# Kernel tuning notes

Hardware: AMD Instinct MI355X
Metric: run time of the kernel (lower is better)

Reference implementation:

```python
import jax, jax.numpy as jnp
import numpy as np

B, S, D, H = 2, 1024, 1024, 8
HD = D // H            # head_dim = 128
NBUCKETS = 64          # bucket_size (number of hash buckets)
NEG = -1e30


def setup_inputs() -> dict:
    key = jax.random.key(0)
    ks = jax.random.split(key, 10)
    scale = D ** -0.5
    return {
        "x": jax.random.normal(ks[0], (B, S, D), dtype=jnp.float32),
        "Wq": jax.random.normal(ks[1], (D, D), dtype=jnp.float32) * scale,
        "bq": jnp.zeros((D,), dtype=jnp.float32),
        "Wk": jax.random.normal(ks[2], (D, D), dtype=jnp.float32) * scale,
        "bk": jnp.zeros((D,), dtype=jnp.float32),
        "Wv": jax.random.normal(ks[3], (D, D), dtype=jnp.float32) * scale,
        "bv": jnp.zeros((D,), dtype=jnp.float32),
        "Wo": jax.random.normal(ks[4], (D, D), dtype=jnp.float32) * scale,
        "bo": jnp.zeros((D,), dtype=jnp.float32),
        "hash_proj": jax.random.normal(ks[5], (H, HD, NBUCKETS), dtype=jnp.float32),
    }


def reference(x, Wq, bq, Wk, bk, Wv, bv, Wo, bo, hash_proj):
    b, s, d = x.shape
    n = b * s  # buckets gather (batch, token) pairs jointly -> flatten batch into tokens

    def split_heads(y):  # [B,S,D] -> [H, B*S, HD]
        return y.reshape(b, s, H, HD).transpose(2, 0, 1, 3).reshape(H, n, HD)

    q = split_heads(x @ Wq + bq)
    k = split_heads(x @ Wk + bk)
    v = split_heads(x @ Wv + bv)

    # learned LSH routing: argmax over hash projections per head
    hash_scores = jnp.einsum('hnd,hdf->hnf', q, hash_proj)
    buckets = jnp.argmax(hash_scores, axis=-1)  # [H, N] int

    # per-bucket attention == masked dense attention with same-bucket mask
    dots = jnp.einsum('hnd,hmd->hnm', q, k) / (HD ** 0.5)  # [H,N,N]
    same = buckets[:, :, None] == buckets[:, None, :]
    attn = jax.nn.softmax(jnp.where(same, dots, NEG), axis=-1)
    o = jnp.einsum('hnm,hmd->hnd', attn, v)  # [H,N,HD]

    out = o.reshape(H, b, s, HD).transpose(1, 2, 0, 3).reshape(b, s, d)
    return out @ Wo + bo
```

## Files before the change

### kernel.cpp

```cpp
#include <hip/hip_runtime.h>
#include <stdint.h>

typedef __attribute__((ext_vector_type(8))) short short8;
typedef __attribute__((ext_vector_type(4))) short short4v;
typedef __attribute__((ext_vector_type(4))) float float4v;
typedef unsigned short u16;

#define N_TOK 2048
#define D_MODEL 1024
#define N_HEAD 8
#define HDIM 128
#define N_BUCKET 64
#define WL_CAP 2048
#define ATTN_BLOCKS 384

__device__ __forceinline__ u16 f2bf(float f) {
  uint32_t u = __float_as_uint(f);
  uint32_t r = u + 0x7fffu + ((u >> 16) & 1u);
  return (u16)(r >> 16);
}
__device__ __forceinline__ float bf2f(u16 h) {
  return __uint_as_float(((uint32_t)h) << 16);
}

__device__ __forceinline__ void async_load16(const void* g, void* l) {
  __builtin_amdgcn_global_load_lds(
      (const __attribute__((address_space(1))) void*)g,
      (__attribute__((address_space(3))) void*)l, 16, 0, 0);
}

__device__ __forceinline__ int xcd_swz(int bid, int nwg) {
  return (bid & 7) * (nwg >> 3) + (bid >> 3);
}

__global__ __launch_bounds__(256) void prep_kernel(
    const float* __restrict__ x, const float* __restrict__ Wq,
    const float* __restrict__ Wk, const float* __restrict__ Wv,
    const float* __restrict__ Wo, const float* __restrict__ proj,
    u16* __restrict__ xhi, u16* __restrict__ xlo,
    u16* __restrict__ wqt_hi, u16* __restrict__ wqt_lo, u16* __restrict__ kvt,
    u16* __restrict__ wot, u16* __restrict__ projt_hi,
    u16* __restrict__ projt_lo) {
  const int z = blockIdx.z;
  if (z == 4) {
    int base = (blockIdx.y * 32 + blockIdx.x) * 2048 + threadIdx.x * 8;
    float4v a = *(const float4v*)&x[base];
    float4v b = *(const float4v*)&x[base + 4];
    short8 hi, lo;
#pragma unroll
    for (int j = 0; j < 4; j++) {
      u16 h = f2bf(a[j]);
      hi[j] = (short)h;
      lo[j] = (short)f2bf(a[j] - bf2f(h));
    }
#pragma unroll
    for (int j = 0; j < 4; j++) {
      u16 h = f2bf(b[j]);
      hi[4 + j] = (short)h;
      lo[4 + j] = (short)f2bf(b[j] - bf2f(h));
    }
    *(short8*)&xhi[base] = hi;
    *(short8*)&xlo[base] = lo;
    return;
  }
  __shared__ float tile[32][33];
  int tx = threadIdx.x & 31, ty = threadIdx.x >> 5;
  if (z == 5) {
    if (blockIdx.x >= 2) return;
    const int head = blockIdx.y >> 2;
    const int r0 = (blockIdx.y & 3) * 32;
    const int c0 = blockIdx.x * 32;
    const float* in = proj + (size_t)head * 128 * 64;
#pragma unroll
    for (int i = 0; i < 4; i++) {
      int rl = ty + i * 8;
      tile[rl][tx] = in[(size_t)(r0 + rl) * 64 + c0 + tx];
    }
    __syncthreads();
#pragma unroll
    for (int i = 0; i < 4; i++) {
      int cl = ty + i * 8;
      float v = tile[tx][cl];
      size_t oidx = (size_t)head * 64 * 128 + (size_t)(c0 + cl) * 128 + r0 + tx;
      u16 h = f2bf(v);
      projt_hi[oidx] = h;
      projt_lo[oidx] = f2bf(v - bf2f(h));
    }
    return;
  }
  const float* in = (z == 0) ? Wq : (z == 1) ? Wk : (z == 2) ? Wv : Wo;
  u16* hi = (z == 0) ? wqt_hi
            : (z == 1) ? kvt
            : (z == 2) ? (kvt + (size_t)1024 * 1024) : wot;
  u16* lo = (z == 0) ? wqt_lo : nullptr;
  const int C = 1024, R = 1024;
  int c0 = blockIdx.x * 32, r0 = blockIdx.y * 32;
#pragma unroll
  for (int i = 0; i < 4; i++) {
    int rl = ty + i * 8;
    tile[rl][tx] = in[(size_t)(r0 + rl) * C + c0 + tx];
  }
  __syncthreads();
#pragma unroll
  for (int i = 0; i < 4; i++) {
    int cl = ty + i * 8;
    float v = tile[tx][cl];
    size_t oidx = (size_t)(c0 + cl) * R + r0 + tx;
    u16 h = f2bf(v);
    hi[oidx] = h;
    if (lo) lo[oidx] = f2bf(v - bf2f(h));
  }
}

template <int BM>
__device__ __forceinline__ void stage_tiles2(const u16* A, const u16* Bt,
                                             u16* As, u16* Bs, int bm, int bn,
                                             int K, int ko, int wave, int lane) {
  const int arow = lane >> 2;
  const int acolb = (lane & 3) * 16;
  constexpr int ACH = BM / 16;
  constexpr int PC = (ACH + 8) / 4;
#pragma unroll
  for (int cc = 0; cc < PC; cc++) {
    int idx = wave * PC + cc;
    if (idx < ACH) {
      int row = idx * 16 + arow;
      const char* g = (const char*)A + ((size_t)(bm + row) * K + ko) * 2 + acolb;
      async_load16(g, (char*)As + idx * 1024);
    } else {
      int row = (idx - ACH) * 16 + arow;
      const char* g = (const char*)Bt + ((size_t)(bn + row) * K + ko) * 2 + acolb;
      async_load16(g, (char*)Bs + (idx - ACH) * 1024);
    }
  }
}

template <int BM>
__global__ __launch_bounds__(256) void gemm_bf16_kernel(
    const u16* __restrict__ A, const u16* __restrict__ Bt,
    float* __restrict__ C, const float* __restrict__ bias,
    const float* __restrict__ bias2, u16* __restrict__ kbf,
    u16* __restrict__ vbf, int N, int K, int flags) {
  constexpr int MI = BM / 32;
  __shared__ __align__(16) u16 As[2][BM * 32];
  __shared__ __align__(16) u16 Bs[2][128 * 32];
  const int tid = threadIdx.x;
  const int wave = tid >> 6, lane = tid & 63;
  const int lhi = lane >> 4, llo = lane & 15;
  const int nbn = N >> 7;
  const int bid = xcd_swz(blockIdx.x, gridDim.x);
  const int bm = (bid / nbn) * BM;
  const int bn = (bid % nbn) << 7;
  const int wm = (BM == 128) ? (wave >> 1) * 64 : (wave & 1) * 32;
  const int wn = (BM == 128) ? (wave & 1) * 64 : (wave >> 1) * 64;

  float4v acc[MI][4];
#pragma unroll
  for (int mi = 0; mi < MI; mi++)
#pragma unroll
    for (int ni = 0; ni < 4; ni++)
#pragma unroll
      for (int r = 0; r < 4; r++) acc[mi][ni][r] = 0.f;

  stage_tiles2<BM>(A, Bt, As[0], Bs[0], bm, bn, K, 0, wave, lane);
  __syncthreads();
  const int nk = K >> 5;
  for (int t = 0; t < nk; t++) {
    const int cur = t & 1;
    if (t + 1 < nk)
      stage_tiles2<BM>(A, Bt, As[cur ^ 1], Bs[cur ^ 1], bm, bn, K,
                       (t + 1) << 5, wave, lane);
    short8 af[MI], bfr[4];
#pragma unroll
    for (int i = 0; i < MI; i++)
      af[i] = *(const short8*)&As[cur][(wm + i * 16 + llo) * 32 + lhi * 8];
#pragma unroll
    for (int i = 0; i < 4; i++)
      bfr[i] = *(const short8*)&Bs[cur][(wn + i * 16 + llo) * 32 + lhi * 8];
#pragma unroll
    for (int mi = 0; mi < MI; mi++)
#pragma unroll
      for (int ni = 0; ni < 4; ni++)
        acc[mi][ni] = __builtin_amdgcn_mfma_f32_16x16x32_bf16(af[mi], bfr[ni],
                                                              acc[mi][ni], 0, 0, 0);
    __syncthreads();
  }

#pragma unroll
  for (int mi = 0; mi < MI; mi++)
#pragma unroll
    for (int ni = 0; ni < 4; ni++) {
      int row0 = bm + wm + mi * 16 + lhi * 4;
      int col = bn + wn + ni * 16 + llo;
      if (flags & 8) {
        u16* dst = (col < 1024) ? kbf : vbf;
        int c = col & 1023;
        float bb = (col < 1024) ? bias[c] : bias2[c];
#pragma unroll
        for (int r = 0; r < 4; r++)
          dst[(size_t)(row0 + r) * 1024 + c] = f2bf(acc[mi][ni][r] + bb);
      } else {
        float bb = (flags & 2) ? bias[col] : 0.f;
        float* cp = C + (size_t)row0 * N + col;
#pragma unroll
        for (int r = 0; r < 4; r++) cp[(size_t)r * N] = acc[mi][ni][r] + bb;
      }
    }
}

#define QROW 136
__global__ __launch_bounds__(256) void proj_gemm_kernel(
    const u16* __restrict__ A0, const u16* __restrict__ A1,
    const u16* __restrict__ B0, const u16* __restrict__ B1,
    const u16* __restrict__ kvt, const u16* __restrict__ projt_hi,
    const u16* __restrict__ projt_lo, const float* __restrict__ bq,
    const float* __restrict__ bk, const float* __restrict__ bv,
    u16* __restrict__ qbb, int* __restrict__ bucket,
    u16* __restrict__ kbf, u16* __restrict__ vbf) {
  __shared__ __align__(16) u16 S3[2][12288];
  const int tid = threadIdx.x;
  const int wave = tid >> 6, lane = tid & 63;
  const int lhi = lane >> 4, llo = lane & 15;
  const int arow = lane >> 2;
  const int acolb = (lane & 3) * 16;
  const int K = 1024;
  const int b = blockIdx.x;
  const int cls = b % 3;

  if (cls == 0) {
    const int bid = b / 3;
    const int bm = (bid >> 3) * 64;
    const int bn = (bid & 7) << 7;
    const int wm = (wave & 1) * 32;
    const int wn = (wave >> 1) * 64;

    float4v acc[2][4];
#pragma unroll
    for (int mi = 0; mi < 2; mi++)
#pragma unroll
      for (int ni = 0; ni < 4; ni++)
#pragma unroll
        for (int r = 0; r < 4; r++) acc[mi][ni][r] = 0.f;

    auto stage = [&](int bb2, int ko) {
      char* base = (char*)&S3[bb2][0];
#pragma unroll
      for (int cc = 0; cc < 6; cc++) {
        int idx = wave * 6 + cc;
        const u16* src;
        int row;
        char* dst;
        if (idx < 4) {
          src = A0; row = bm + idx * 16 + arow; dst = base + idx * 1024;
        } else if (idx < 8) {
          src = A1; row = bm + (idx - 4) * 16 + arow; dst = base + 4096 + (idx - 4) * 1024;
        } else if (idx < 16) {
          src = B0; row = bn + (idx - 8) * 16 + arow; dst = base + 8192 + (idx - 8) * 1024;
        } else {
          src = B1; row = bn + (idx - 16) * 16 + arow; dst = base + 16384 + (idx - 16) * 1024;
        }
        async_load16((const char*)src + ((size_t)row * K + ko) * 2 + acolb, dst);
      }
    };

    stage(0, 0);
    __syncthreads();
    for (int t = 0; t < 32; t++) {
      const int cur = t & 1;
      if (t + 1 < 32) stage(cur ^ 1, (t + 1) << 5);
      const u16* Sc = &S3[cur][0];
      short8 afh[2], afl[2], bfh[4], bfl[4];
#pragma unroll
      for (int i = 0; i < 2; i++) {
        afh[i] = *(const short8*)&Sc[(wm + i * 16 + llo) * 32 + lhi * 8];
        afl[i] = *(const short8*)&Sc[2048 + (wm + i * 16 + llo) * 32 + lhi * 8];
      }
#pragma unroll
      for (int i = 0; i < 4; i++) {
        bfh[i] = *(const short8*)&Sc[4096 + (wn + i * 16 + llo) * 32 + lhi * 8];
        bfl[i] = *(const short8*)&Sc[8192 + (wn + i * 16 + llo) * 32 + lhi * 8];
      }
#pragma unroll
      for (int mi = 0; mi < 2; mi++)
#pragma unroll
        for (int ni = 0; ni < 4; ni++)
          acc[mi][ni] = __builtin_amdgcn_mfma_f32_16x16x32_bf16(afh[mi], bfh[ni],
                                                                acc[mi][ni], 0, 0, 0);
#pragma unroll
      for (int mi = 0; mi < 2; mi++)
#pragma unroll
        for (int ni = 0; ni < 4; ni++)
          acc[mi][ni] = __builtin_amdgcn_mfma_f32_16x16x32_bf16(afh[mi], bfl[ni],
                                                                acc[mi][ni], 0, 0, 0);
#pragma unroll
      for (int mi = 0; mi < 2; mi++)
#pragma unroll
        for (int ni = 0; ni < 4; ni++)
          acc[mi][ni] = __builtin_amdgcn_mfma_f32_16x16x32_bf16(afl[mi], bfh[ni],
                                                                acc[mi][ni], 0, 0, 0);
      __syncthreads();
    }

    u16* sQh = &S3[0][0];
    u16* sQl = &S3[0][64 * QROW];
#pragma unroll
    for (int mi = 0; mi < 2; mi++)
#pragma unroll
      for (int ni = 0; ni < 4; ni++) {
        int rl0 = wm + mi * 16 + lhi * 4;
        int col = wn + ni * 16 + llo;
        float bb = bq[bn + col];
#pragma unroll
        for (int r = 0; r < 4; r++) {
          float v = acc[mi][ni][r] + bb;
          u16 h = f2bf(v);
          qbb[(size_t)(bm + rl0 + r) * 1024 + bn + col] = h;
          sQh[(rl0 + r) * QROW + col] = h;
          sQl[(rl0 + r) * QROW + col] = f2bf(v - bf2f(h));
        }
      }
    __syncthreads();

    {
      const int h = bn >> 7;
      const int wm2 = wave * 16;
      short8 qh[4], ql[4];
#pragma unroll
      for (int kf = 0; kf < 4; kf++) {
        qh[kf] = *(const short8*)&sQh[(wm2 + llo) * QROW + kf * 32 + lhi * 8];
        ql[kf] = *(const short8*)&sQl[(wm2 + llo) * QROW + kf * 32 + lhi * 8];
      }
      const u16* ph = projt_hi + (size_t)h * 64 * 128;
      const u16* pl = projt_lo + (size_t)h * 64 * 128;
      float4v sc2[4];
#pragma unroll
      for (int nf = 0; nf < 4; nf++)
#pragma unroll
        for (int r = 0; r < 4; r++) sc2[nf][r] = 0.f;
#pragma unroll
      for (int nf = 0; nf < 4; nf++) {
        int brow = (nf * 16 + llo) * 128;
#pragma unroll
        for (int kf = 0; kf < 4; kf++) {
          short8 bh = *(const short8*)&ph[brow + kf * 32 + lhi * 8];
          short8 bl = *(const short8*)&pl[brow + kf * 32 + lhi * 8];
          sc2[nf] = __builtin_amdgcn_mfma_f32_16x16x32_bf16(qh[kf], bh, sc2[nf], 0, 0, 0);
          sc2[nf] = __builtin_amdgcn_mfma_f32_16x16x32_bf16(qh[kf], bl, sc2[nf], 0, 0, 0);
          sc2[nf] = __builtin_amdgcn_mfma_f32_16x16x32_bf16(ql[kf], bh, sc2[nf], 0, 0, 0);
        }
      }
#pragma unroll
      for (int r = 0; r < 4; r++) {
        float best = sc2[0][r];
        int bi = llo;
#pragma unroll
        for (int nf = 1; nf < 4; nf++) {
          float v = sc2[nf][r];
          if (v > best) { best = v; bi = nf * 16 + llo; }
        }
#pragma unroll
        for (int o = 1; o < 16; o <<= 1) {
          float ov = __shfl_xor(best, o);
          int oi = __shfl_xor(bi, o);
          if (ov > best || (ov == best && oi < bi)) { best = ov; bi = oi; }
        }
        if (llo == 0) bucket[h * N_TOK + bm + wm2 + lhi * 4 + r] = bi;
      }
    }
  } else {
    const int bid2 = (b / 3) * 2 + (cls - 1);
    const int bm = (bid2 >> 4) * 64;
    const int bn = (bid2 & 15) << 7;
    const int wm = (wave & 1) * 32;
    const int wn = (wave >> 1) * 64;

    float4v acc[2][4];
#pragma unroll
    for (int mi = 0; mi < 2; mi++)
#pragma unroll
      for (int ni = 0; ni < 4; ni++)
#pragma unroll
        for (int r = 0; r < 4; r++) acc[mi][ni][r] = 0.f;

    stage_tiles2<64>(A0, kvt, &S3[0][0], &S3[0][4096], bm, bn, K, 0, wave, lane);
    __syncthreads();
    for (int t = 0; t < 32; t++) {
      const int cur = t & 1;
      if (t + 1 < 32)
        stage_tiles2<64>(A0, kvt, &S3[0][(cur ^ 1) * 2048],
                         &S3[0][4096 + (cur ^ 1) * 4096], bm, bn, K,
                         (t + 1) << 5, wave, lane);
      const u16* Ac = &S3[0][cur * 2048];
      const u16* Bc = &S3[0][4096 + cur * 4096];
      short8 af[2], bfr[4];
#pragma unroll
      for (int i = 0; i < 2; i++)
        af[i] = *(const short8*)&Ac[(wm + i * 16 + llo) * 32 + lhi * 8];
#pragma unroll
      for (int i = 0; i < 4; i++)
        bfr[i] = *(const short8*)&Bc[(wn + i * 16 + llo) * 32 + lhi * 8];
#pragma unroll
      for (int mi = 0; mi < 2; mi++)
#pragma unroll
        for (int ni = 0; ni < 4; ni++)
          acc[mi][ni] = __builtin_amdgcn_mfma_f32_16x16x32_bf16(af[mi], bfr[ni],
                                                                acc[mi][ni], 0, 0, 0);
      __syncthreads();
    }

#pragma unroll
    for (int mi = 0; mi < 2; mi++)
#pragma unroll
      for (int ni = 0; ni < 4; ni++) {
        int row0 = bm + wm + mi * 16 + lhi * 4;
        int col = bn + wn + ni * 16 + llo;
        u16* dst = (col < 1024) ? kbf : vbf;
        int c = col & 1023;
        float bb = (col < 1024) ? bk[c] : bv[c];
#pragma unroll
        for (int r = 0; r < 4; r++)
          dst[(size_t)(row0 + r) * 1024 + c] = f2bf(acc[mi][ni][r] + bb);
      }
  }
}

__global__ __launch_bounds__(64) void bucket_count_kernel(
    const int* __restrict__ bucket, int* __restrict__ counts) {
  int hb = blockIdx.x;
  int h = hb >> 6, b = hb & 63;
  int lane = threadIdx.x;
  int cnt = 0;
  for (int t = 0; t < N_TOK; t += 64) {
    bool match = bucket[h * N_TOK + t + lane] == b;
    unsigned long long mask = __ballot(match);
    cnt += __popcll(mask);
  }
  if (lane == 0) counts[hb] = cnt;
}

__global__ __launch_bounds__(512) void build_wl_kernel(
    const int* __restrict__ counts, int* __restrict__ offsets,
    int* __restrict__ wl, int* __restrict__ wl_count) {
  __shared__ int sc[512];
  int tid = threadIdx.x;
  int cnt = counts[tid];
  sc[tid] = cnt;
  __syncthreads();
  for (int o = 1; o < 512; o <<= 1) {
    int v = (tid >= o) ? sc[tid - o] : 0;
    __syncthreads();
    sc[tid] += v;
    __syncthreads();
  }
  offsets[tid] = sc[tid] - cnt;
  __syncthreads();
  int nq = (cnt + 15) >> 4;
  sc[tid] = nq;
  __syncthreads();
  for (int o = 1; o < 512; o <<= 1) {
    int v = (tid >= o) ? sc[tid - o] : 0;
    __syncthreads();
    sc[tid] += v;
    __syncthreads();
  }
  int base = sc[tid] - nq;
  int h = tid >> 6, b = tid & 63;
  for (int i = 0; i < nq; i++) wl[base + i] = (h << 13) | (b << 7) | i;
  if (tid == 511) wl_count[0] = sc[511];
}

__global__ __launch_bounds__(64) void bucket_fill_kernel(
    const int* __restrict__ bucket, const int* __restrict__ offsets,
    int* __restrict__ perm) {
  int hb = blockIdx.x;
  int h = hb >> 6, b = hb & 63;
  int lane = threadIdx.x;
  int base = offsets[hb];
  for (int t = 0; t < N_TOK; t += 64) {
    int tok = t + lane;
    bool match = bucket[h * N_TOK + tok] == b;
    unsigned long long mask = __ballot(match);
    if (match) {
      int pos = base + __popcll(mask & ((1ull << lane) - 1ull));
      perm[pos] = tok;
    }
    base += __popcll(mask);
  }
}

__global__ __launch_bounds__(256) void gather_vt_kernel(
    const u16* __restrict__ vbb, const int* __restrict__ perm,
    u16* __restrict__ Vts) {
  __shared__ u16 lds[64][72];
  int bid = blockIdx.x;
  int h = bid >> 6;
  int ptile = (bid & 63) >> 1;
  int d0 = (bid & 1) * 64;
  int pos0 = ptile * 64;
  int t = threadIdx.x;
#pragma unroll
  for (int i = 0; i < 2; i++) {
    int unit = t + 256 * i;
    int p = unit >> 3, seg = unit & 7;
    int tok = perm[h * N_TOK + pos0 + p];
    short8 v = *(const short8*)&vbb[(size_t)tok * D_MODEL + h * HDIM + d0 + seg * 8];
    *(short8*)&lds[p][seg * 8] = v;
  }
  __syncthreads();
#pragma unroll
  for (int i = 0; i < 8; i++) {
    int unit = t + 256 * i;
    int drow = unit >> 5, pp = unit & 31;
    uint32_t val = (uint32_t)lds[2 * pp][drow] |
                   ((uint32_t)lds[2 * pp + 1][drow] << 16);
    uint32_t* dst = (uint32_t*)&Vts[(size_t)(h * HDIM + d0 + drow) * N_TOK + pos0];
    dst[pp] = val;
  }
}

__global__ __launch_bounds__(256) void attn_bucket_kernel(
    const u16* __restrict__ qbb, const u16* __restrict__ kbb,
    const u16* __restrict__ Vts, const int* __restrict__ perm,
    const int* __restrict__ offsets, const int* __restrict__ counts,
    const int* __restrict__ wl, const int* __restrict__ wl_count,
    u16* __restrict__ ob) {
  const int wave = threadIdx.x >> 6, lane = threadIdx.x & 63;
  const int lhi = lane >> 4, llo = lane & 15;
  const int wslot = blockIdx.x * 4 + wave;
  const int NW = ATTN_BLOCKS * 4;
  const int cnt = wl_count[0];
  __shared__ __align__(16) u16 P_lds[4][16][64];
  const float scale = 0.08838834764831845f;

  for (int e = wslot; e < cnt; e += NW) {
    int ent = wl[e];
    int h = ent >> 13, qt = ent & 127;
    int hb = (h << 6) | ((ent >> 7) & 63);
    int off = offsets[hb];
    int bs = counts[hb];
    int offh = off - h * N_TOK;
    int qbase = qt * 16;

    int qr = qbase + llo;
    int tokq = perm[off + min(qr, bs - 1)];
    const u16* qrow = &qbb[(size_t)tokq * D_MODEL + h * HDIM];
    short8 qf[4];
#pragma unroll
    for (int kf = 0; kf < 4; kf++)
      qf[kf] = *(const short8*)&qrow[kf * 32 + lhi * 8];

    float m[4], l[4];
#pragma unroll
    for (int r = 0; r < 4; r++) { m[r] = -INFINITY; l[r] = 0.f; }
    float4v accO[8];
#pragma unroll
    for (int d = 0; d < 8; d++)
#pragma unroll
      for (int r = 0; r < 4; r++) accO[d][r] = 0.f;

    for (int c0 = 0; c0 < bs; c0 += 64) {
      float4v scv[4];
#pragma unroll
      for (int nf = 0; nf < 4; nf++)
#pragma unroll
        for (int r = 0; r < 4; r++) scv[nf][r] = 0.f;
#pragma unroll
      for (int nf = 0; nf < 4; nf++) {
        int kcol = c0 + nf * 16 + llo;
        int tokk = perm[off + min(kcol, bs - 1)];
        const u16* krow = &kbb[(size_t)tokk * D_MODEL + h * HDIM];
#pragma unroll
        for (int kf = 0; kf < 4; kf++) {
          short8 kfr = *(const short8*)&krow[kf * 32 + lhi * 8];
          scv[nf] = __builtin_amdgcn_mfma_f32_16x16x32_bf16(qf[kf], kfr, scv[nf], 0, 0, 0);
        }
      }

      float tmax[4];
#pragma unroll
      for (int r = 0; r < 4; r++) tmax[r] = -INFINITY;
#pragma unroll
      for (int nf = 0; nf < 4; nf++) {
        bool valid = (c0 + nf * 16 + llo) < bs;
#pragma unroll
        for (int r = 0; r < 4; r++) {
          float v = valid ? scv[nf][r] * scale : -1e30f;
          scv[nf][r] = v;
          tmax[r] = fmaxf(tmax[r], v);
        }
      }
#pragma unroll
      for (int r = 0; r < 4; r++)
#pragma unroll
        for (int o = 1; o < 16; o <<= 1)
          tmax[r] = fmaxf(tmax[r], __shfl_xor(tmax[r], o));

      float resc[4], psum[4];
#pragma unroll
      for (int r = 0; r < 4; r++) {
        float mn = fmaxf(m[r], tmax[r]);
        resc[r] = __expf(m[r] - mn);
        m[r] = mn;
        psum[r] = 0.f;
      }
#pragma unroll
      for (int nf = 0; nf < 4; nf++)
#pragma unroll
        for (int r = 0; r < 4; r++) {
          float p = __expf(scv[nf][r] - m[r]);
          psum[r] += p;
          P_lds[wave][lhi * 4 + r][nf * 16 + llo] = f2bf(p);
        }
#pragma unroll
      for (int r = 0; r < 4; r++) {
#pragma unroll
        for (int o = 1; o < 16; o <<= 1) psum[r] += __shfl_xor(psum[r], o);
        l[r] = l[r] * resc[r] + psum[r];
      }
#pragma unroll
      for (int d = 0; d < 8; d++)
#pragma unroll
        for (int r = 0; r < 4; r++) accO[d][r] *= resc[r];

      asm volatile("s_waitcnt lgkmcnt(0)" ::: "memory");
      short8 pf[2];
#pragma unroll
      for (int k2 = 0; k2 < 2; k2++)
        pf[k2] = *(const short8*)&P_lds[wave][llo][k2 * 32 + lhi * 8];
#pragma unroll
      for (int d = 0; d < 8; d++)
#pragma unroll
        for (int k2 = 0; k2 < 2; k2++) {
          short8 vfr = *(const short8*)&Vts[(size_t)(h * HDIM + d * 16 + llo) * N_TOK +
                                            offh + c0 + k2 * 32 + lhi * 8];
          accO[d] = __builtin_amdgcn_mfma_f32_16x16x32_bf16(pf[k2], vfr, accO[d], 0, 0, 0);
        }
      asm volatile("" ::: "memory");
    }

#pragma unroll
    for (int r = 0; r < 4; r++) {
      int rl = qbase + lhi * 4 + r;
      if (rl < bs) {
        int tok = perm[off + rl];
        float inv = 1.f / l[r];
#pragma unroll
        for (int d = 0; d < 8; d++)
          ob[(size_t)tok * D_MODEL + h * HDIM + d * 16 + llo] = f2bf(accO[d][r] * inv);
      }
    }
  }
}

extern "C" void kernel_launch(void* const* d_in, const int* in_sizes, int n_in,
                              void* d_out, int out_size, void* d_ws, size_t ws_size,
                              hipStream_t stream) {
  const float* x  = (const float*)d_in[0];
  const float* Wq = (const float*)d_in[1];
  const float* bq = (const float*)d_in[2];
  const float* Wk = (const float*)d_in[3];
  const float* bk = (const float*)d_in[4];
  const float* Wv = (const float*)d_in[5];
  const float* bv = (const float*)d_in[6];
  const float* Wo = (const float*)d_in[7];
  const float* bo = (const float*)d_in[8];
  const float* hp = (const float*)d_in[9];
  float* out = (float*)d_out;

  char* ws = (char*)d_ws;
  size_t off = 0;
  auto alloc = [&](size_t b) {
    char* p = ws + off;
    off += (b + 255) & ~(size_t)255;
    return p;
  };

  const int N = N_TOK, D = D_MODEL;
  u16* xhi    = (u16*)alloc((size_t)N * D * 2);
  u16* xlo    = (u16*)alloc((size_t)N * D * 2);
  u16* wqt_hi = (u16*)alloc((size_t)D * D * 2);
  u16* wqt_lo = (u16*)alloc((size_t)D * D * 2);
  u16* kvt    = (u16*)alloc((size_t)2 * D * D * 2);
  u16* wot    = (u16*)alloc((size_t)D * D * 2);
  u16* pjt_hi = (u16*)alloc((size_t)N_HEAD * 64 * 128 * 2);
  u16* pjt_lo = (u16*)alloc((size_t)N_HEAD * 64 * 128 * 2);
  u16* qbb    = (u16*)alloc((size_t)N * D * 2);
  u16* kbb    = (u16*)alloc((size_t)N * D * 2);
  u16* vbb    = (u16*)alloc((size_t)N * D * 2);
  u16* Vts    = (u16*)alloc((size_t)N_HEAD * HDIM * N * 2 + 256);
  int* bucket = (int*)alloc((size_t)N_HEAD * N * 4);
  int* counts = (int*)alloc(512 * 4);
  int* offs   = (int*)alloc(512 * 4);
  int* perm   = (int*)alloc((size_t)N_HEAD * N * 4);
  int* wl     = (int*)alloc(WL_CAP * 4);
  int* wlcnt  = (int*)alloc(256);
  u16* ob     = (u16*)alloc((size_t)N * D * 2);

  prep_kernel<<<dim3(32, 32, 6), 256, 0, stream>>>(
      x, Wq, Wk, Wv, Wo, hp, xhi, xlo, wqt_hi, wqt_lo, kvt, wot, pjt_hi, pjt_lo);

  proj_gemm_kernel<<<768, 256, 0, stream>>>(
      xhi, xlo, wqt_hi, wqt_lo, kvt, pjt_hi, pjt_lo, bq, bk, bv,
      qbb, bucket, kbb, vbb);

  bucket_count_kernel<<<512, 64, 0, stream>>>(bucket, counts);
  build_wl_kernel<<<1, 512, 0, stream>>>(counts, offs, wl, wlcnt);
  bucket_fill_kernel<<<512, 64, 0, stream>>>(bucket, offs, perm);
  gather_vt_kernel<<<512, 256, 0, stream>>>(vbb, perm, Vts);

  attn_bucket_kernel<<<ATTN_BLOCKS, 256, 0, stream>>>(
      qbb, kbb, Vts, perm, offs, counts, wl, wlcnt, ob);

  gemm_bf16_kernel<64><<<(N / 64) * (D / 128), 256, 0, stream>>>(
      ob, wot, out, bo, nullptr, nullptr, nullptr, D, D, 2);

  (void)in_sizes; (void)n_in; (void)out_size; (void)ws_size;
}
```

Measured before the change: 109.8 us.

## Fuse bucket counting into projection GEMM and merge scan with bucket fill

Bucket histogram counts are now produced with atomics inside the projection GEMM's argmax epilogue, with the counts zeroed by spare prep blocks. The separate scan and fill kernels are merged into one, where each block computes its own prefix offsets from the 512 counts. This removes two kernel launches and one full pass over the bucket array. In exchange it adds atomic contention and redundant prefix sums in every block.

```diff
diff --git a/kernel.cpp b/kernel.cpp
--- a/kernel.cpp
+++ b/kernel.cpp
@@ -40,7 +40,7 @@
     u16* __restrict__ xhi, u16* __restrict__ xlo,
     u16* __restrict__ wqt_hi, u16* __restrict__ wqt_lo, u16* __restrict__ kvt,
     u16* __restrict__ wot, u16* __restrict__ projt_hi,
-    u16* __restrict__ projt_lo) {
+    u16* __restrict__ projt_lo, int* __restrict__ counts) {
   const int z = blockIdx.z;
   if (z == 4) {
     int base = (blockIdx.y * 32 + blockIdx.x) * 2048 + threadIdx.x * 8;
@@ -66,7 +66,14 @@
   __shared__ float tile[32][33];
   int tx = threadIdx.x & 31, ty = threadIdx.x >> 5;
   if (z == 5) {
-    if (blockIdx.x >= 2) return;
+    if (blockIdx.x == 2) {
+      if (blockIdx.y == 0) {
+        counts[threadIdx.x] = 0;
+        counts[threadIdx.x + 256] = 0;
+      }
+      return;
+    }
+    if (blockIdx.x > 2) return;
     const int head = blockIdx.y >> 2;
     const int r0 = (blockIdx.y & 3) * 32;
     const int c0 = blockIdx.x * 32;
@@ -216,7 +223,7 @@
     const u16* __restrict__ projt_lo, const float* __restrict__ bq,
     const float* __restrict__ bk, const float* __restrict__ bv,
     u16* __restrict__ qbb, int* __restrict__ bucket,
-    u16* __restrict__ kbf, u16* __restrict__ vbf) {
+    u16* __restrict__ kbf, u16* __restrict__ vbf, int* __restrict__ counts) {
   __shared__ __align__(16) u16 S3[2][12288];
   const int tid = threadIdx.x;
   const int wave = tid >> 6, lane = tid & 63;
@@ -364,7 +371,10 @@
           int oi = __shfl_xor(bi, o);
           if (ov > best || (ov == best && oi < bi)) { best = ov; bi = oi; }
         }
-        if (llo == 0) bucket[h * N_TOK + bm + wm2 + lhi * 4 + r] = bi;
+        if (llo == 0) {
+          bucket[h * N_TOK + bm + wm2 + lhi * 4 + r] = bi;
+          atomicAdd(&counts[h * 64 + bi], 1);
+        }
       }
     }
   } else {
@@ -424,58 +434,32 @@
   }
 }
 
-__global__ __launch_bounds__(64) void bucket_count_kernel(
-    const int* __restrict__ bucket, int* __restrict__ counts) {
-  int hb = blockIdx.x;
-  int h = hb >> 6, b = hb & 63;
-  int lane = threadIdx.x;
-  int cnt = 0;
-  for (int t = 0; t < N_TOK; t += 64) {
-    bool match = bucket[h * N_TOK + t + lane] == b;
-    unsigned long long mask = __ballot(match);
-    cnt += __popcll(mask);
-  }
-  if (lane == 0) counts[hb] = cnt;
-}
-
-__global__ __launch_bounds__(512) void build_wl_kernel(
-    const int* __restrict__ counts, int* __restrict__ offsets,
+__global__ __launch_bounds__(64) void fillwl_kernel(
+    const int* __restrict__ bucket, const int* __restrict__ counts,
+    int* __restrict__ offsets_g, int* __restrict__ perm,
     int* __restrict__ wl, int* __restrict__ wl_count) {
-  __shared__ int sc[512];
-  int tid = threadIdx.x;
-  int cnt = counts[tid];
-  sc[tid] = cnt;
-  __syncthreads();
-  for (int o = 1; o < 512; o <<= 1) {
-    int v = (tid >= o) ? sc[tid - o] : 0;
-    __syncthreads();
-    sc[tid] += v;
-    __syncthreads();
-  }
-  offsets[tid] = sc[tid] - cnt;
-  __syncthreads();
-  int nq = (cnt + 15) >> 4;
-  sc[tid] = nq;
-  __syncthreads();
-  for (int o = 1; o < 512; o <<= 1) {
-    int v = (tid >= o) ? sc[tid - o] : 0;
-    __syncthreads();
-    sc[tid] += v;
-    __syncthreads();
-  }
-  int base = sc[tid] - nq;
-  int h = tid >> 6, b = tid & 63;
-  for (int i = 0; i < nq; i++) wl[base + i] = (h << 13) | (b << 7) | i;
-  if (tid == 511) wl_count[0] = sc[511];
-}
-
-__global__ __launch_bounds__(64) void bucket_fill_kernel(
-    const int* __restrict__ bucket, const int* __restrict__ offsets,
-    int* __restrict__ perm) {
-  int hb = blockIdx.x;
-  int h = hb >> 6, b = hb & 63;
-  int lane = threadIdx.x;
-  int base = offsets[hb];
+  const int hb = blockIdx.x;
+  const int h = hb >> 6, b = hb & 63;
+  const int lane = threadIdx.x;
+  int offp = 0, wlp = 0;
+#pragma unroll
+  for (int i = 0; i < 8; i++) {
+    int idx = i * 64 + lane;
+    int c = counts[idx];
+    int nq = (c + 15) >> 4;
+    if (idx < hb) { offp += c; wlp += nq; }
+  }
+#pragma unroll
+  for (int o = 1; o < 64; o <<= 1) {
+    offp += __shfl_xor(offp, o);
+    wlp += __shfl_xor(wlp, o);
+  }
+  const int cnt = counts[hb];
+  const int nq = (cnt + 15) >> 4;
+  if (lane == 0) offsets_g[hb] = offp;
+  for (int i = lane; i < nq; i += 64) wl[wlp + i] = (h << 13) | (b << 7) | i;
+  if (hb == 511 && lane == 0) wl_count[0] = wlp + nq;
+  int base = offp;
   for (int t = 0; t < N_TOK; t += 64) {
     int tok = t + lane;
     bool match = bucket[h * N_TOK + tok] == b;
@@ -697,15 +681,14 @@
   u16* ob     = (u16*)alloc((size_t)N * D * 2);
 
   prep_kernel<<<dim3(32, 32, 6), 256, 0, stream>>>(
-      x, Wq, Wk, Wv, Wo, hp, xhi, xlo, wqt_hi, wqt_lo, kvt, wot, pjt_hi, pjt_lo);
+      x, Wq, Wk, Wv, Wo, hp, xhi, xlo, wqt_hi, wqt_lo, kvt, wot, pjt_hi,
+      pjt_lo, counts);
 
   proj_gemm_kernel<<<768, 256, 0, stream>>>(
       xhi, xlo, wqt_hi, wqt_lo, kvt, pjt_hi, pjt_lo, bq, bk, bv,
-      qbb, bucket, kbb, vbb);
-
-  bucket_count_kernel<<<512, 64, 0, stream>>>(bucket, counts);
-  build_wl_kernel<<<1, 512, 0, stream>>>(counts, offs, wl, wlcnt);
-  bucket_fill_kernel<<<512, 64, 0, stream>>>(bucket, offs, perm);
+      qbb, bucket, kbb, vbb, counts);
+
+  fillwl_kernel<<<512, 64, 0, stream>>>(bucket, counts, offs, perm, wl, wlcnt);
   gather_vt_kernel<<<512, 256, 0, stream>>>(vbb, perm, Vts);
 
   attn_bucket_kernel<<<ATTN_BLOCKS, 256, 0, stream>>>(
```

Result: slower. 114.2 us (+4.1%).
